# Kernel tuning notes

Measured on AMD Instinct MI355X. Metric: run time of the kernel, lower is better.

## Reference

```python
import jax, jax.numpy as jnp
import numpy as np

N, V, C, H, W, P = 4, 5, 128, 128, 128, 4096
IMG_W, IMG_H = 1920.0, 1080.0
FM = 128.0


def setup_inputs() -> dict:
    key = jax.random.key(0)
    k1, k2, k3, k4 = jax.random.split(key, 4)
    feature_maps = jax.random.normal(k1, (N, V, C, H, W), jnp.float32)
    xy = jax.random.uniform(k2, (N, P, 2), jnp.float32, -800.0, 800.0)
    z = jax.random.uniform(k3, (N, P, 1), jnp.float32, 100.0, 2000.0)
    extra = jax.random.uniform(k4, (N, P, 2), jnp.float32)
    sample_points = jnp.concatenate([xy, z, extra], axis=-1)  # [N,P,5]
    R = jnp.tile(jnp.eye(3, dtype=jnp.float32), (N, V, 1, 1))
    T = jnp.tile(jnp.array([0.0, 0.0, -3000.0], jnp.float32), (N, V, 1))
    f = jnp.full((N, V, 2), 1200.0, jnp.float32)
    c = jnp.tile(jnp.array([IMG_W / 2, IMG_H / 2], jnp.float32), (N, V, 1))
    k = jnp.zeros((N, V, 3), jnp.float32)  # radial distortion
    p = jnp.zeros((N, V, 2), jnp.float32)  # tangential distortion
    # affine transform (from get_affine_transform): full image -> feature map
    trans = jnp.tile(jnp.array([[FM / IMG_W, 0.0, 0.0], [0.0, FM / IMG_H, 0.0]], jnp.float32), (N, V, 1, 1))
    wh = jnp.tile(jnp.array([IMG_W, IMG_H], jnp.float32), (N, V, 1))
    fm_size = jnp.array([FM, FM], jnp.float32)
    return dict(feature_maps=feature_maps, sample_points=sample_points, R=R, T=T,
                f=f, c=c, k=k, p=p, trans=trans, wh=wh, fm_size=fm_size)


def _grid_sample_one(img, grid):
    # img: [C,H,W], grid: [P,2] in normalized coords; bilinear, zeros padding, align_corners=True
    Ci, Hi, Wi = img.shape
    x = (grid[:, 0] + 1.0) * 0.5 * (Wi - 1)
    y = (grid[:, 1] + 1.0) * 0.5 * (Hi - 1)
    x0 = jnp.floor(x); y0 = jnp.floor(y)
    wx1 = x - x0; wx0 = 1.0 - wx1
    wy1 = y - y0; wy0 = 1.0 - wy1

    def gather(xi, yi):
        valid = (xi >= 0) & (xi <= Wi - 1) & (yi >= 0) & (yi <= Hi - 1)
        xc = jnp.clip(xi, 0, Wi - 1).astype(jnp.int32)
        yc = jnp.clip(yi, 0, Hi - 1).astype(jnp.int32)
        return img[:, yc, xc] * valid.astype(img.dtype)  # [C,P]

    return (gather(x0, y0) * (wx0 * wy0) + gather(x0 + 1, y0) * (wx1 * wy0)
            + gather(x0, y0 + 1) * (wx0 * wy1) + gather(x0 + 1, y0 + 1) * (wx1 * wy1))


def _forward(feature_maps, sample_points, R, T, f, c, k, p, trans, wh, fm_size):
    n, v, ch, h, w = feature_maps.shape
    pts = sample_points[:, :, :3]  # [N,P,3]
    # world -> camera: X_cam = R @ (X - T)
    Xc = jnp.einsum('nvij,nvpj->nvpi', R, pts[:, None, :, :] - T[:, :, None, :])  # [N,V,P,3]
    xn = Xc[..., 0] / Xc[..., 2]
    yn = Xc[..., 1] / Xc[..., 2]
    r2 = xn * xn + yn * yn
    k1 = k[..., 0:1]; k2 = k[..., 1:2]; k3 = k[..., 2:3]
    p1 = p[..., 0:1]; p2 = p[..., 1:2]
    radial = 1.0 + k1 * r2 + k2 * r2 * r2 + k3 * r2 * r2 * r2
    xd = xn * radial + 2.0 * p1 * xn * yn + p2 * (r2 + 2.0 * xn * xn)
    yd = yn * radial + p1 * (r2 + 2.0 * yn * yn) + 2.0 * p2 * xn * yn
    xy = jnp.stack([xd, yd], -1) * f[:, :, None, :] + c[:, :, None, :]  # [N,V,P,2] pixel coords
    width = wh[..., 0:1]; height = wh[..., 1:2]
    bound = ((xy[..., 0] >= 0) & (xy[..., 1] >= 0)
             & (xy[..., 0] < width) & (xy[..., 1] < height)).astype(feature_maps.dtype)  # [N,V,P]
    max_wh = jnp.maximum(wh[..., 0], wh[..., 1])[:, :, None, None]
    pix = jnp.clip(xy, -1.0, max_wh)
    # affine transform to feature-map coords
    pix_t = jnp.einsum('nvij,nvpj->nvpi', trans[..., :2], pix) + trans[..., 2][:, :, None, :]
    norm = jnp.clip(pix_t / (fm_size - 1.0) * 2.0 - 1.0, -1.1, 1.1)  # [N,V,P,2]
    sampled = jax.vmap(_grid_sample_one)(feature_maps.reshape(n * v, ch, h, w),
                                         norm.reshape(n * v, -1, 2))  # [NV,C,P]
    sampled = sampled.reshape(n, v, ch, -1)
    feats = (sampled * bound[:, :, None, :]).transpose(0, 3, 1, 2)  # [N,P,V,C]
    is_not_nan = jnp.logical_not(jnp.isnan(feats).any(axis=(2, 3)))  # [N,P]
    bounding = (bound.sum(axis=1) > 0) & is_not_nan  # discard_nan=False path
    return feats, bounding


def reference(feature_maps, sample_points, R, T, f, c, k, p, trans, wh, fm_size):
    feats, bounding = _forward(feature_maps, sample_points, R, T, f, c, k, p, trans, wh, fm_size)
    return feats, bounding, sample_points
```

## Files before the change

### kernel.cpp

```cpp
#include <hip/hip_runtime.h>
#include <math.h>

#define N 4
#define V 5
#define C 128
#define H 128
#define W 128
#define P 4096
#define HW (H * W)
#define PTS 16

typedef float  fvec4 __attribute__((ext_vector_type(4)));
typedef unsigned short usvec4 __attribute__((ext_vector_type(4)));

__device__ __forceinline__ unsigned short f2bf_rne(float x) {
    unsigned u = __float_as_uint(x);
    unsigned rounding = 0x7fffu + ((u >> 16) & 1u);
    return (unsigned short)((u + rounding) >> 16);
}
__device__ __forceinline__ float bf2f(unsigned short b) {
    return __uint_as_float(((unsigned)b) << 16);
}

__global__ __launch_bounds__(256) void transpose_kernel(
    const float* __restrict__ fm, unsigned short* __restrict__ fmT)
{
    const int nv  = blockIdx.y;
    const int hw0 = blockIdx.x * 64;
    __shared__ float lds[64][C + 1];

    const int t = threadIdx.x;

    {
        const int hwl = (t & 15) * 4;
        const int cb  = t >> 4;
        const float* src = fm + (size_t)nv * C * HW + hw0 + hwl;
        for (int c = cb; c < C; c += 16) {
            const fvec4 v = __builtin_nontemporal_load(
                (const fvec4*)(src + (size_t)c * HW));
            lds[hwl + 0][c] = v.x;
            lds[hwl + 1][c] = v.y;
            lds[hwl + 2][c] = v.z;
            lds[hwl + 3][c] = v.w;
        }
    }
    __syncthreads();

    {
        const int c4 = (t & 31) * 4;
        unsigned short* dst = fmT + ((size_t)nv * HW + hw0) * C + c4;
        for (int hw = (t >> 5); hw < 64; hw += 8) {
            const fvec4 v = *(const fvec4*)&lds[hw][c4];
            usvec4 o;
            o.x = f2bf_rne(v.x);
            o.y = f2bf_rne(v.y);
            o.z = f2bf_rne(v.z);
            o.w = f2bf_rne(v.w);
            *(usvec4*)(dst + (size_t)hw * C) = o;
        }
    }
}

__global__ __launch_bounds__(256) void project_sample_kernel(
    const unsigned short* __restrict__ fmT,
    const float* __restrict__ sp,
    const float* __restrict__ Rm,
    const float* __restrict__ Tm,
    const float* __restrict__ fv,
    const float* __restrict__ cv,
    const float* __restrict__ kv,
    const float* __restrict__ pv,
    const float* __restrict__ trans,
    const float* __restrict__ wh,
    const float* __restrict__ fmsz,
    float* __restrict__ out_feats,
    float* __restrict__ out_bound,
    float* __restrict__ out_sp)
{
    const int pb = blockIdx.x;
    const int n  = pb >> 8;
    const int p0 = (pb & 255) * PTS;
    const int t  = threadIdx.x;
    const int base_pt = n * P + p0;

    __shared__ int   s_idx[PTS * V][4];
    __shared__ float s_w[PTS * V][4];
    __shared__ float s_bnd[PTS * V];
    __shared__ int   s_nan[PTS];

    if (t < PTS) s_nan[t] = 0;
    if (t < PTS * 5) out_sp[base_pt * 5 + t] = sp[base_pt * 5 + t];

    if (t < PTS * V) {
        const int pt = t / V;
        const int v  = t - pt * V;
        const int nv = n * V + v;

        const float X = sp[(base_pt + pt) * 5 + 0];
        const float Y = sp[(base_pt + pt) * 5 + 1];
        const float Z = sp[(base_pt + pt) * 5 + 2];

        const float* Rv = Rm + nv * 9;
        const float tx = Tm[nv * 3 + 0], ty = Tm[nv * 3 + 1], tz = Tm[nv * 3 + 2];
        const float px = X - tx, py = Y - ty, pz = Z - tz;
        const float Xc0 = Rv[0] * px + Rv[1] * py + Rv[2] * pz;
        const float Xc1 = Rv[3] * px + Rv[4] * py + Rv[5] * pz;
        const float Xc2 = Rv[6] * px + Rv[7] * py + Rv[8] * pz;
        const float xn = Xc0 / Xc2;
        const float yn = Xc1 / Xc2;
        const float r2 = xn * xn + yn * yn;
        const float k1 = kv[nv * 3 + 0], k2 = kv[nv * 3 + 1], k3 = kv[nv * 3 + 2];
        const float p1 = pv[nv * 2 + 0], p2 = pv[nv * 2 + 1];
        const float radial = 1.0f + k1 * r2 + k2 * r2 * r2 + k3 * r2 * r2 * r2;
        const float xd = xn * radial + 2.0f * p1 * xn * yn + p2 * (r2 + 2.0f * xn * xn);
        const float yd = yn * radial + p1 * (r2 + 2.0f * yn * yn) + 2.0f * p2 * xn * yn;
        const float xy0 = xd * fv[nv * 2 + 0] + cv[nv * 2 + 0];
        const float xy1 = yd * fv[nv * 2 + 1] + cv[nv * 2 + 1];
        const float width  = wh[nv * 2 + 0];
        const float height = wh[nv * 2 + 1];
        const bool bound = (xy0 >= 0.0f) && (xy1 >= 0.0f) && (xy0 < width) && (xy1 < height);
        const float maxwh = fmaxf(width, height);
        const float pix0 = fminf(fmaxf(xy0, -1.0f), maxwh);
        const float pix1 = fminf(fmaxf(xy1, -1.0f), maxwh);
        const float* tr = trans + nv * 6;
        const float pt0 = tr[0] * pix0 + tr[1] * pix1 + tr[2];
        const float pt1 = tr[3] * pix0 + tr[4] * pix1 + tr[5];
        const float fm0 = fmsz[0], fm1 = fmsz[1];
        float g0 = pt0 / (fm0 - 1.0f) * 2.0f - 1.0f;
        float g1 = pt1 / (fm1 - 1.0f) * 2.0f - 1.0f;
        g0 = fminf(fmaxf(g0, -1.1f), 1.1f);
        g1 = fminf(fmaxf(g1, -1.1f), 1.1f);

        const float xg = (g0 + 1.0f) * 0.5f * (float)(W - 1);
        const float yg = (g1 + 1.0f) * 0.5f * (float)(H - 1);
        const float x0f = floorf(xg), y0f = floorf(yg);
        const float wx1 = xg - x0f, wx0 = 1.0f - wx1;
        const float wy1 = yg - y0f, wy0 = 1.0f - wy1;
        const int x0 = (int)x0f, y0 = (int)y0f;
        const int x1 = x0 + 1,  y1 = y0 + 1;
        const bool vx0 = (x0 >= 0) && (x0 <= W - 1);
        const bool vx1 = (x1 >= 0) && (x1 <= W - 1);
        const bool vy0 = (y0 >= 0) && (y0 <= H - 1);
        const bool vy1 = (y1 >= 0) && (y1 <= H - 1);
        const int x0c = min(max(x0, 0), W - 1);
        const int x1c = min(max(x1, 0), W - 1);
        const int y0c = min(max(y0, 0), H - 1);
        const int y1c = min(max(y1, 0), H - 1);

        s_idx[t][0] = y0c * W + x0c;
        s_idx[t][1] = y0c * W + x1c;
        s_idx[t][2] = y1c * W + x0c;
        s_idx[t][3] = y1c * W + x1c;
        s_w[t][0] = (vx0 && vy0) ? (wx0 * wy0) : 0.0f;
        s_w[t][1] = (vx1 && vy0) ? (wx1 * wy0) : 0.0f;
        s_w[t][2] = (vx0 && vy1) ? (wx0 * wy1) : 0.0f;
        s_w[t][3] = (vx1 && vy1) ? (wx1 * wy1) : 0.0f;
        s_bnd[t] = bound ? 1.0f : 0.0f;
    }
    __syncthreads();

    {
        const int grp = t >> 5;
        const int c4  = (t & 31) * 4;
        const unsigned short* img_n = fmT + (size_t)(n * V) * HW * C;
        #pragma unroll 2
        for (int i = grp; i < PTS * V; i += 8) {
            const int pt = i / V;
            const int v  = i - pt * V;
            const unsigned short* img = img_n + (size_t)v * HW * C + c4;
            const usvec4 b00 = *(const usvec4*)(img + (size_t)s_idx[i][0] * C);
            const usvec4 b10 = *(const usvec4*)(img + (size_t)s_idx[i][1] * C);
            const usvec4 b01 = *(const usvec4*)(img + (size_t)s_idx[i][2] * C);
            const usvec4 b11 = *(const usvec4*)(img + (size_t)s_idx[i][3] * C);
            const float w00 = s_w[i][0], w10 = s_w[i][1];
            const float w01 = s_w[i][2], w11 = s_w[i][3];
            const float bnd = s_bnd[i];
            fvec4 f;
            f.x = (bf2f(b00.x) * w00 + bf2f(b10.x) * w10
                 + bf2f(b01.x) * w01 + bf2f(b11.x) * w11) * bnd;
            f.y = (bf2f(b00.y) * w00 + bf2f(b10.y) * w10
                 + bf2f(b01.y) * w01 + bf2f(b11.y) * w11) * bnd;
            f.z = (bf2f(b00.z) * w00 + bf2f(b10.z) * w10
                 + bf2f(b01.z) * w01 + bf2f(b11.z) * w11) * bnd;
            f.w = (bf2f(b00.w) * w00 + bf2f(b10.w) * w10
                 + bf2f(b01.w) * w01 + bf2f(b11.w) * w11) * bnd;
            if ((f.x != f.x) | (f.y != f.y) | (f.z != f.z) | (f.w != f.w))
                s_nan[pt] = 1;
            __builtin_nontemporal_store(
                f, (fvec4*)&out_feats[((size_t)(base_pt + pt) * V + v) * C + c4]);
        }
    }
    __syncthreads();

    if (t < PTS) {
        bool any_b = false;
        #pragma unroll
        for (int v = 0; v < V; ++v) any_b |= (s_bnd[t * V + v] != 0.0f);
        out_bound[base_pt + t] = (any_b && (s_nan[t] == 0)) ? 1.0f : 0.0f;
    }
}

extern "C" void kernel_launch(void* const* d_in, const int* in_sizes, int n_in,
                              void* d_out, int out_size, void* d_ws, size_t ws_size,
                              hipStream_t stream) {
    const float* fm    = (const float*)d_in[0];
    const float* sp    = (const float*)d_in[1];
    const float* Rm    = (const float*)d_in[2];
    const float* Tm    = (const float*)d_in[3];
    const float* fv    = (const float*)d_in[4];
    const float* cv    = (const float*)d_in[5];
    const float* kv    = (const float*)d_in[6];
    const float* pv    = (const float*)d_in[7];
    const float* trans = (const float*)d_in[8];
    const float* wh    = (const float*)d_in[9];
    const float* fmsz  = (const float*)d_in[10];

    float* out        = (float*)d_out;
    float* out_feats  = out;
    float* out_bound  = out + (size_t)N * P * V * C;
    float* out_sp     = out_bound + (size_t)N * P;

    unsigned short* fmT = (unsigned short*)d_ws;

    dim3 tgrid(HW / 64, N * V);
    transpose_kernel<<<tgrid, 256, 0, stream>>>(fm, fmT);

    project_sample_kernel<<<N * (P / PTS), 256, 0, stream>>>(
        fmT, sp, Rm, Tm, fv, cv, kv, pv, trans, wh, fmsz,
        out_feats, out_bound, out_sp);
}
```

Before: 287.8 us.

## Compute sample bounding boxes first and transpose only the touched feature-map tiles

Projection moves into its own kernel that runs first. It writes the bilinear indices, weights and bound flags to workspace, and it reduces a per-view bounding box of the sampled pixel coordinates. The transpose kernel reads that box and skips 32-pixel row tiles that no sample touches, so it no longer reads and converts the whole fp32 feature map. This costs an extra launch and a round trip for the indices and weights through global memory, and the saving depends on how spread out the projected points are.

```diff
diff --git a/kernel.cpp b/kernel.cpp
--- a/kernel.cpp
+++ b/kernel.cpp
@@ -9,6 +9,8 @@
 #define P 4096
 #define HW (H * W)
 #define PTS 16
+#define PCH 8
+#define PPB (P / PCH)
 
 typedef float  fvec4 __attribute__((ext_vector_type(4)));
 typedef unsigned short usvec4 __attribute__((ext_vector_type(4)));
@@ -22,47 +24,7 @@
     return __uint_as_float(((unsigned)b) << 16);
 }
 
-__global__ __launch_bounds__(256) void transpose_kernel(
-    const float* __restrict__ fm, unsigned short* __restrict__ fmT)
-{
-    const int nv  = blockIdx.y;
-    const int hw0 = blockIdx.x * 64;
-    __shared__ float lds[64][C + 1];
-
-    const int t = threadIdx.x;
-
-    {
-        const int hwl = (t & 15) * 4;
-        const int cb  = t >> 4;
-        const float* src = fm + (size_t)nv * C * HW + hw0 + hwl;
-        for (int c = cb; c < C; c += 16) {
-            const fvec4 v = __builtin_nontemporal_load(
-                (const fvec4*)(src + (size_t)c * HW));
-            lds[hwl + 0][c] = v.x;
-            lds[hwl + 1][c] = v.y;
-            lds[hwl + 2][c] = v.z;
-            lds[hwl + 3][c] = v.w;
-        }
-    }
-    __syncthreads();
-
-    {
-        const int c4 = (t & 31) * 4;
-        unsigned short* dst = fmT + ((size_t)nv * HW + hw0) * C + c4;
-        for (int hw = (t >> 5); hw < 64; hw += 8) {
-            const fvec4 v = *(const fvec4*)&lds[hw][c4];
-            usvec4 o;
-            o.x = f2bf_rne(v.x);
-            o.y = f2bf_rne(v.y);
-            o.z = f2bf_rne(v.z);
-            o.w = f2bf_rne(v.w);
-            *(usvec4*)(dst + (size_t)hw * C) = o;
-        }
-    }
-}
-
-__global__ __launch_bounds__(256) void project_sample_kernel(
-    const unsigned short* __restrict__ fmT,
+__global__ __launch_bounds__(256) void project_kernel(
     const float* __restrict__ sp,
     const float* __restrict__ Rm,
     const float* __restrict__ Tm,
@@ -73,59 +35,61 @@
     const float* __restrict__ trans,
     const float* __restrict__ wh,
     const float* __restrict__ fmsz,
-    float* __restrict__ out_feats,
-    float* __restrict__ out_bound,
-    float* __restrict__ out_sp)
+    int4*   __restrict__ ws_idx,
+    float4* __restrict__ ws_w,
+    float*  __restrict__ ws_bnd,
+    int4*   __restrict__ ws_bbox)
 {
-    const int pb = blockIdx.x;
-    const int n  = pb >> 8;
-    const int p0 = (pb & 255) * PTS;
+    const int nv = blockIdx.x;
+    const int ch = blockIdx.y;
+    const int n  = nv / V;
     const int t  = threadIdx.x;
-    const int base_pt = n * P + p0;
-
-    __shared__ int   s_idx[PTS * V][4];
-    __shared__ float s_w[PTS * V][4];
-    __shared__ float s_bnd[PTS * V];
-    __shared__ int   s_nan[PTS];
-
-    if (t < PTS) s_nan[t] = 0;
-    if (t < PTS * 5) out_sp[base_pt * 5 + t] = sp[base_pt * 5 + t];
-
-    if (t < PTS * V) {
-        const int pt = t / V;
-        const int v  = t - pt * V;
-        const int nv = n * V + v;
-
-        const float X = sp[(base_pt + pt) * 5 + 0];
-        const float Y = sp[(base_pt + pt) * 5 + 1];
-        const float Z = sp[(base_pt + pt) * 5 + 2];
-
-        const float* Rv = Rm + nv * 9;
-        const float tx = Tm[nv * 3 + 0], ty = Tm[nv * 3 + 1], tz = Tm[nv * 3 + 2];
+
+    const float* Rv = Rm + nv * 9;
+    const float R0 = Rv[0], R1 = Rv[1], R2 = Rv[2];
+    const float R3 = Rv[3], R4 = Rv[4], R5 = Rv[5];
+    const float R6 = Rv[6], R7 = Rv[7], R8 = Rv[8];
+    const float tx = Tm[nv * 3 + 0], ty = Tm[nv * 3 + 1], tz = Tm[nv * 3 + 2];
+    const float fx = fv[nv * 2 + 0], fy = fv[nv * 2 + 1];
+    const float cx = cv[nv * 2 + 0], cy = cv[nv * 2 + 1];
+    const float k1 = kv[nv * 3 + 0], k2 = kv[nv * 3 + 1], k3 = kv[nv * 3 + 2];
+    const float p1 = pv[nv * 2 + 0], p2 = pv[nv * 2 + 1];
+    const float* tr = trans + nv * 6;
+    const float t0 = tr[0], t1 = tr[1], t2 = tr[2];
+    const float t3 = tr[3], t4 = tr[4], t5 = tr[5];
+    const float width  = wh[nv * 2 + 0];
+    const float height = wh[nv * 2 + 1];
+    const float maxwh  = fmaxf(width, height);
+    const float fm0 = fmsz[0], fm1 = fmsz[1];
+    const int v = nv - n * V;
+
+    int minx = W - 1, maxx = 0, miny = H - 1, maxy = 0;
+
+    #pragma unroll
+    for (int k = 0; k < PPB / 256; ++k) {
+        const int p  = ch * PPB + k * 256 + t;
+        const int gp = n * P + p;
+        const float X = sp[gp * 5 + 0];
+        const float Y = sp[gp * 5 + 1];
+        const float Z = sp[gp * 5 + 2];
+
         const float px = X - tx, py = Y - ty, pz = Z - tz;
-        const float Xc0 = Rv[0] * px + Rv[1] * py + Rv[2] * pz;
-        const float Xc1 = Rv[3] * px + Rv[4] * py + Rv[5] * pz;
-        const float Xc2 = Rv[6] * px + Rv[7] * py + Rv[8] * pz;
+        const float Xc0 = R0 * px + R1 * py + R2 * pz;
+        const float Xc1 = R3 * px + R4 * py + R5 * pz;
+        const float Xc2 = R6 * px + R7 * py + R8 * pz;
         const float xn = Xc0 / Xc2;
         const float yn = Xc1 / Xc2;
         const float r2 = xn * xn + yn * yn;
-        const float k1 = kv[nv * 3 + 0], k2 = kv[nv * 3 + 1], k3 = kv[nv * 3 + 2];
-        const float p1 = pv[nv * 2 + 0], p2 = pv[nv * 2 + 1];
         const float radial = 1.0f + k1 * r2 + k2 * r2 * r2 + k3 * r2 * r2 * r2;
         const float xd = xn * radial + 2.0f * p1 * xn * yn + p2 * (r2 + 2.0f * xn * xn);
         const float yd = yn * radial + p1 * (r2 + 2.0f * yn * yn) + 2.0f * p2 * xn * yn;
-        const float xy0 = xd * fv[nv * 2 + 0] + cv[nv * 2 + 0];
-        const float xy1 = yd * fv[nv * 2 + 1] + cv[nv * 2 + 1];
-        const float width  = wh[nv * 2 + 0];
-        const float height = wh[nv * 2 + 1];
+        const float xy0 = xd * fx + cx;
+        const float xy1 = yd * fy + cy;
         const bool bound = (xy0 >= 0.0f) && (xy1 >= 0.0f) && (xy0 < width) && (xy1 < height);
-        const float maxwh = fmaxf(width, height);
         const float pix0 = fminf(fmaxf(xy0, -1.0f), maxwh);
         const float pix1 = fminf(fmaxf(xy1, -1.0f), maxwh);
-        const float* tr = trans + nv * 6;
-        const float pt0 = tr[0] * pix0 + tr[1] * pix1 + tr[2];
-        const float pt1 = tr[3] * pix0 + tr[4] * pix1 + tr[5];
-        const float fm0 = fmsz[0], fm1 = fmsz[1];
+        const float pt0 = t0 * pix0 + t1 * pix1 + t2;
+        const float pt1 = t3 * pix0 + t4 * pix1 + t5;
         float g0 = pt0 / (fm0 - 1.0f) * 2.0f - 1.0f;
         float g1 = pt1 / (fm1 - 1.0f) * 2.0f - 1.0f;
         g0 = fminf(fmaxf(g0, -1.1f), 1.1f);
@@ -147,15 +111,114 @@
         const int y0c = min(max(y0, 0), H - 1);
         const int y1c = min(max(y1, 0), H - 1);
 
-        s_idx[t][0] = y0c * W + x0c;
-        s_idx[t][1] = y0c * W + x1c;
-        s_idx[t][2] = y1c * W + x0c;
-        s_idx[t][3] = y1c * W + x1c;
-        s_w[t][0] = (vx0 && vy0) ? (wx0 * wy0) : 0.0f;
-        s_w[t][1] = (vx1 && vy0) ? (wx1 * wy0) : 0.0f;
-        s_w[t][2] = (vx0 && vy1) ? (wx0 * wy1) : 0.0f;
-        s_w[t][3] = (vx1 && vy1) ? (wx1 * wy1) : 0.0f;
-        s_bnd[t] = bound ? 1.0f : 0.0f;
+        ws_idx[(size_t)gp * V + v] = make_int4(
+            y0c * W + x0c, y0c * W + x1c, y1c * W + x0c, y1c * W + x1c);
+        ws_w[(size_t)gp * V + v] = make_float4(
+            (vx0 && vy0) ? (wx0 * wy0) : 0.0f,
+            (vx1 && vy0) ? (wx1 * wy0) : 0.0f,
+            (vx0 && vy1) ? (wx0 * wy1) : 0.0f,
+            (vx1 && vy1) ? (wx1 * wy1) : 0.0f);
+        ws_bnd[(size_t)gp * V + v] = bound ? 1.0f : 0.0f;
+
+        minx = min(minx, x0c); maxx = max(maxx, x1c);
+        miny = min(miny, y0c); maxy = max(maxy, y1c);
+    }
+
+    __shared__ int ra[256], rb[256], rc[256], rd[256];
+    ra[t] = minx; rb[t] = maxx; rc[t] = miny; rd[t] = maxy;
+    __syncthreads();
+    for (int s = 128; s > 0; s >>= 1) {
+        if (t < s) {
+            ra[t] = min(ra[t], ra[t + s]);
+            rb[t] = max(rb[t], rb[t + s]);
+            rc[t] = min(rc[t], rc[t + s]);
+            rd[t] = max(rd[t], rd[t + s]);
+        }
+        __syncthreads();
+    }
+    if (t == 0) ws_bbox[nv * PCH + ch] = make_int4(ra[0], rb[0], rc[0], rd[0]);
+}
+
+__global__ __launch_bounds__(256) void transpose_kernel(
+    const float* __restrict__ fm, unsigned short* __restrict__ fmT,
+    const int4* __restrict__ ws_bbox)
+{
+    const int nv   = blockIdx.y;
+    const int tile = blockIdx.x;
+    const int y  = tile >> 2;
+    const int xq = (tile & 3) * 32;
+
+    int minx = W - 1, maxx = 0, miny = H - 1, maxy = 0;
+    const int4* bb = ws_bbox + nv * PCH;
+    #pragma unroll
+    for (int i = 0; i < PCH; ++i) {
+        const int4 b = bb[i];
+        minx = min(minx, b.x); maxx = max(maxx, b.y);
+        miny = min(miny, b.z); maxy = max(maxy, b.w);
+    }
+    if (y < miny || y > maxy || xq > maxx || xq + 31 < minx) return;
+
+    __shared__ float lds[32][C + 1];
+    const int t   = threadIdx.x;
+    const int hw0 = y * W + xq;
+
+    {
+        const int hwl = (t & 7) * 4;
+        const int cb  = t >> 3;
+        const float* src = fm + (size_t)nv * C * HW + hw0 + hwl;
+        for (int c = cb; c < C; c += 32) {
+            const fvec4 vv = __builtin_nontemporal_load(
+                (const fvec4*)(src + (size_t)c * HW));
+            lds[hwl + 0][c] = vv.x;
+            lds[hwl + 1][c] = vv.y;
+            lds[hwl + 2][c] = vv.z;
+            lds[hwl + 3][c] = vv.w;
+        }
+    }
+    __syncthreads();
+
+    {
+        const int c4 = (t & 31) * 4;
+        unsigned short* dst = fmT + ((size_t)nv * HW + hw0) * C + c4;
+        for (int hw = (t >> 5); hw < 32; hw += 8) {
+            const fvec4 vv = *(const fvec4*)&lds[hw][c4];
+            usvec4 o;
+            o.x = f2bf_rne(vv.x);
+            o.y = f2bf_rne(vv.y);
+            o.z = f2bf_rne(vv.z);
+            o.w = f2bf_rne(vv.w);
+            *(usvec4*)(dst + (size_t)hw * C) = o;
+        }
+    }
+}
+
+__global__ __launch_bounds__(256) void sample_kernel(
+    const unsigned short* __restrict__ fmT,
+    const float* __restrict__ sp,
+    const int4*   __restrict__ ws_idx,
+    const float4* __restrict__ ws_w,
+    const float*  __restrict__ ws_bnd,
+    float* __restrict__ out_feats,
+    float* __restrict__ out_bound,
+    float* __restrict__ out_sp)
+{
+    const int pb = blockIdx.x;
+    const int n  = pb >> 8;
+    const int p0 = (pb & 255) * PTS;
+    const int t  = threadIdx.x;
+    const int base_pt = n * P + p0;
+
+    __shared__ int4   s_idx[PTS * V];
+    __shared__ float4 s_w[PTS * V];
+    __shared__ float  s_bnd[PTS * V];
+    __shared__ int    s_nan[PTS];
+
+    if (t < PTS) s_nan[t] = 0;
+    if (t < PTS * 5) out_sp[base_pt * 5 + t] = sp[base_pt * 5 + t];
+    if (t < PTS * V) {
+        s_idx[t] = ws_idx[(size_t)base_pt * V + t];
+        s_w[t]   = ws_w[(size_t)base_pt * V + t];
+        s_bnd[t] = ws_bnd[(size_t)base_pt * V + t];
     }
     __syncthreads();
 
@@ -168,12 +231,13 @@
             const int pt = i / V;
             const int v  = i - pt * V;
             const unsigned short* img = img_n + (size_t)v * HW * C + c4;
-            const usvec4 b00 = *(const usvec4*)(img + (size_t)s_idx[i][0] * C);
-            const usvec4 b10 = *(const usvec4*)(img + (size_t)s_idx[i][1] * C);
-            const usvec4 b01 = *(const usvec4*)(img + (size_t)s_idx[i][2] * C);
-            const usvec4 b11 = *(const usvec4*)(img + (size_t)s_idx[i][3] * C);
-            const float w00 = s_w[i][0], w10 = s_w[i][1];
-            const float w01 = s_w[i][2], w11 = s_w[i][3];
+            const int4 ix = s_idx[i];
+            const usvec4 b00 = *(const usvec4*)(img + (size_t)ix.x * C);
+            const usvec4 b10 = *(const usvec4*)(img + (size_t)ix.y * C);
+            const usvec4 b01 = *(const usvec4*)(img + (size_t)ix.z * C);
+            const usvec4 b11 = *(const usvec4*)(img + (size_t)ix.w * C);
+            const float4 wv = s_w[i];
+            const float w00 = wv.x, w10 = wv.y, w01 = wv.z, w11 = wv.w;
             const float bnd = s_bnd[i];
             fvec4 f;
             f.x = (bf2f(b00.x) * w00 + bf2f(b10.x) * w10
@@ -220,12 +284,20 @@
     float* out_bound  = out + (size_t)N * P * V * C;
     float* out_sp     = out_bound + (size_t)N * P;
 
-    unsigned short* fmT = (unsigned short*)d_ws;
-
-    dim3 tgrid(HW / 64, N * V);
-    transpose_kernel<<<tgrid, 256, 0, stream>>>(fm, fmT);
-
-    project_sample_kernel<<<N * (P / PTS), 256, 0, stream>>>(
-        fmT, sp, Rm, Tm, fv, cv, kv, pv, trans, wh, fmsz,
-        out_feats, out_bound, out_sp);
-}
+    char* ws = (char*)d_ws;
+    unsigned short* fmT = (unsigned short*)ws;
+    size_t off = (size_t)N * V * HW * C * sizeof(unsigned short);
+    int4* ws_idx = (int4*)(ws + off);   off += (size_t)N * P * V * sizeof(int4);
+    float4* ws_w = (float4*)(ws + off); off += (size_t)N * P * V * sizeof(float4);
+    float* ws_bnd = (float*)(ws + off); off += (size_t)N * P * V * sizeof(float);
+    int4* ws_bbox = (int4*)(ws + off);
+
+    project_kernel<<<dim3(N * V, PCH), 256, 0, stream>>>(
+        sp, Rm, Tm, fv, cv, kv, pv, trans, wh, fmsz,
+        ws_idx, ws_w, ws_bnd, ws_bbox);
+
+    transpose_kernel<<<dim3(HW / 32, N * V), 256, 0, stream>>>(fm, fmT, ws_bbox);
+
+    sample_kernel<<<N * (P / PTS), 256, 0, stream>>>(
+        fmT, sp, ws_idx, ws_w, ws_bnd, out_feats, out_bound, out_sp);
+}
```

After: 266.1 us. 1.08x faster.
